# Kernel tuning notes

Hardware: AMD Instinct MI355X
Metric: run time of the kernel (lower is better)

Reference implementation:

```python
import jax, jax.numpy as jnp
import numpy as np

N, M, C, L, T = 1024, 64, 512, 64, 8192
EPS = 1e-16


def setup_inputs() -> dict:
    key = jax.random.key(0)
    ks = jax.random.split(key, 9)
    sc = 0.05
    return {
        "sequence": jax.random.uniform(ks[0], (T, L), dtype=jnp.float32),
        "Wc": jax.random.normal(ks[1], (L + M, C), jnp.float32) * sc,
        "bc": jnp.zeros((C,), jnp.float32),
        "Wr": jax.random.normal(ks[2], (C, M + 6), jnp.float32) * sc,
        "br": jnp.zeros((M + 6,), jnp.float32),
        "Ww": jax.random.normal(ks[3], (C, 3 * M + 6), jnp.float32) * sc,
        "bw": jnp.zeros((3 * M + 6,), jnp.float32),
        "Wo": jax.random.normal(ks[4], (M, L), jnp.float32) * sc,
        "bo": jnp.zeros((L,), jnp.float32),
    }


def _address(Mt, k, beta, g, sh, gamma, w_prev):
    # content addressing: cosine similarity of key against each memory row
    sim = (Mt @ k) / (jnp.linalg.norm(Mt, axis=1) * jnp.linalg.norm(k) + EPS)
    wc = jax.nn.softmax(beta * sim)                      # [N]
    wg = g * wc + (1.0 - g) * w_prev                     # interpolation
    # circular convolution with 3-tap shift kernel (-1, 0, +1)
    ws = sh[0] * jnp.roll(wg, 1) + sh[1] * wg + sh[2] * jnp.roll(wg, -1)
    wsh = ws ** gamma                                    # sharpening
    return wsh / (jnp.sum(wsh) + EPS)


def _head_params(o):
    k = jnp.tanh(o[:M])
    beta = jax.nn.softplus(o[M])
    g = jax.nn.sigmoid(o[M + 1])
    sh = jax.nn.softmax(o[M + 2:M + 5])
    gamma = 1.0 + jax.nn.softplus(o[M + 5])
    return k, beta, g, sh, gamma


def reference(sequence, Wc, bc, Wr, br, Ww, bw, Wo, bo):
    M0 = jnp.full((N, M), 1e-06, jnp.float32)            # memory_bias
    w0 = jnp.zeros((N,), jnp.float32).at[N // 2].set(1.0)  # weight_bias
    r0 = jnp.full((M,), 1e-06, jnp.float32)              # read_bias

    def step(carry, s):
        Mt, ww, rw, r = carry
        h = jnp.tanh(jnp.concatenate([s, r]) @ Wc + bc)  # controller
        # write head: k, beta, g, shift, gamma, erase, add
        ow = h @ Ww + bw
        k, beta, g, sh, gamma = _head_params(ow)
        e = jax.nn.sigmoid(ow[M + 6:2 * M + 6])
        a = jnp.tanh(ow[2 * M + 6:])
        ww_n = _address(Mt, k, beta, g, sh, gamma, ww)
        Mt = Mt * (1.0 - ww_n[:, None] * e[None, :]) + ww_n[:, None] * a[None, :]
        # read head
        orr = h @ Wr + br
        k, beta, g, sh, gamma = _head_params(orr)
        rw_n = _address(Mt, k, beta, g, sh, gamma, rw)
        r_n = rw_n @ Mt                                  # [M]
        s_out = jnp.clip(r_n @ Wo + bo, 0.0, 1.0)
        return (Mt, ww_n, rw_n, r_n), (s_out, ww_n, rw_n, a, r_n)

    _, (seq_out, ww_h, rw_h, a_h, r_h) = jax.lax.scan(step, (M0, w0, w0, r0), sequence)
    return seq_out, ww_h, rw_h, a_h, r_h
```

## Files before the change

kernel.cpp:

```cpp
#include <hip/hip_runtime.h>
#include <math.h>

#define NN 1024
#define MM 64
#define CC 512
#define LL 64
#define TT 8192
#define EPSF 1e-16f

#define OFF_SEQ 0
#define OFF_WW  (TT*LL)
#define OFF_RW  (OFF_WW + TT*NN)
#define OFF_A   (OFF_RW + TT*NN)
#define OFF_R   (OFF_A + TT*MM)

#define WSF_PRE   0
#define WSF_M     (TT*CC)
#define WSF_WCAT  (WSF_M + 32768)

#define BAR() asm volatile("s_waitcnt lgkmcnt(0)\n\ts_barrier" ::: "memory")

__device__ __forceinline__ float sigmoid_f(float x) { return 1.0f / (1.0f + __expf(-x)); }
__device__ __forceinline__ float softplus_f(float x) { return (x > 15.0f) ? x : __logf(1.0f + __expf(x)); }
__device__ __forceinline__ float tanh_f(float x) { float e = __expf(2.0f * x); return 1.0f - 2.0f / (e + 1.0f); }
__device__ __forceinline__ float pow_f(float b, float g) { return __expf(g * __logf(b)); }
__device__ __forceinline__ int bitrev4(int l) {
    return ((l & 1) << 3) | ((l & 2) << 1) | ((l & 4) >> 1) | ((l & 8) >> 3);
}

__device__ __forceinline__ float xor_any(float v, const int m, const int lane) {
    if (m == 1)
        return __int_as_float(__builtin_amdgcn_mov_dpp(__float_as_int(v), 0xB1, 0xF, 0xF, true));
    if (m == 2)
        return __int_as_float(__builtin_amdgcn_mov_dpp(__float_as_int(v), 0x4E, 0xF, 0xF, true));
    return __shfl_xor(v, m, 64);
}

__device__ __forceinline__ float bfly64(float s, const int lane) {
    s += xor_any(s, 1, lane);
    s += xor_any(s, 2, lane);
    s += xor_any(s, 4, lane);
    s += xor_any(s, 8, lane);
    s += xor_any(s, 16, lane);
    s += xor_any(s, 32, lane);
    return s;
}

__global__ void pre_kernel(const float* __restrict__ seq, const float* __restrict__ Wc,
                           const float* __restrict__ bc, float* __restrict__ pre) {
    int gid = blockIdx.x * blockDim.x + threadIdx.x;
    int t = gid >> 9;
    int j = gid & 511;
    if (t >= TT) return;
    const float* s = seq + t * LL;
    float acc = bc[j];
    #pragma unroll 8
    for (int i = 0; i < LL; ++i) acc += s[i] * Wc[i * CC + j];
    pre[gid] = acc;
}

__global__ void pack_kernel(const float* __restrict__ Ww, const float* __restrict__ Wr,
                            float* __restrict__ Wcat) {
    int gid = blockIdx.x * 256 + threadIdx.x;
    if (gid >= 512 * 272) return;
    int r = gid / 272, c = gid - r * 272;
    float v = 0.0f;
    if (c < 198) v = Ww[r * 198 + c];
    else if (c < 268) v = Wr[r * 70 + (c - 198)];
    Wcat[gid] = v;
}

__global__ __launch_bounds__(1024)
void ntm_kernel(
    const float* __restrict__ pre,
    const float* __restrict__ Wc,
    const float* __restrict__ Wcat,
    const float* __restrict__ br,
    const float* __restrict__ bw,
    const float* __restrict__ Wo,
    const float* __restrict__ bo,
    float* __restrict__ out)
{
    __shared__ __align__(16) float sh_part[4096];
    __shared__ __align__(16) float sh_h[CC];
    __shared__ __align__(16) float sh_kw[MM];
    __shared__ __align__(16) float sh_kr[MM];
    __shared__ __align__(16) float sh_e[MM];
    __shared__ __align__(16) float sh_a[MM];
    __shared__ __align__(16) float sh_scal[16];
    __shared__ __align__(16) float sh_evbuf[NN];
    __shared__ __align__(16) float sh_wpbuf[NN];
    __shared__ __align__(16) float red[4][16];
    __shared__ __align__(16) float wmat[16][MM];
    __shared__ __align__(16) float sh_r[MM];
    __shared__ __align__(16) float sh_WoT[LL * MM];
    __shared__ __align__(16) float sh_bo[LL];
    __shared__ __align__(16) float sh_bw[200];
    __shared__ __align__(16) float sh_br[72];
    __shared__ __align__(16) float sh_pren[CC];

    const int tid  = threadIdx.x;
    const int lane = tid & 63;
    const int wv   = tid >> 6;

    for (int idx = tid; idx < MM * LL; idx += NN) {
        int i = idx >> 6, o = idx & 63;
        sh_WoT[o * MM + i] = Wo[i * LL + o];
    }
    if (tid < LL)  sh_bo[tid] = bo[tid];
    if (tid < 198) sh_bw[tid] = bw[tid];
    if (tid < 70)  sh_br[tid] = br[tid];
    if (tid < MM)  sh_r[tid] = 1e-6f;
    if (tid < CC)  sh_pren[tid] = pre[tid];

    float Mlo[32];
    #pragma unroll
    for (int j = 0; j < 32; ++j) Mlo[j] = 1e-6f;
    float4 mh[8];
    #pragma unroll
    for (int k = 0; k < 8; ++k) mh[k] = make_float4(1e-6f, 1e-6f, 1e-6f, 1e-6f);
    float rown = sqrtf(64.0f * 1e-12f);
    float wwprev = (tid == NN / 2) ? 1.0f : 0.0f;
    float rwprev = wwprev;
    __syncthreads();

    for (int t = 0; t < TT; ++t) {
        {
            int g = tid & 127, q = tid >> 7;
            const float4* wbase = (const float4*)(Wc + (64 + q * 8) * CC) + g;
            float4 ra = *(const float4*)(sh_r + q * 8);
            float4 rb = *(const float4*)(sh_r + q * 8 + 4);
            float rv[8] = {ra.x, ra.y, ra.z, ra.w, rb.x, rb.y, rb.z, rb.w};
            float4 acc = make_float4(0.0f, 0.0f, 0.0f, 0.0f);
            #pragma unroll
            for (int i = 0; i < 8; ++i) {
                float4 w = wbase[i * 128];
                acc.x += rv[i] * w.x; acc.y += rv[i] * w.y;
                acc.z += rv[i] * w.z; acc.w += rv[i] * w.w;
            }
            ((float4*)sh_part)[q * 128 + g] = acc;
        }
        BAR();
        if (tid < CC) {
            float p0 = sh_part[tid]          + sh_part[512 + tid];
            float p1 = sh_part[1024 + tid]   + sh_part[1536 + tid];
            float p2 = sh_part[2048 + tid]   + sh_part[2560 + tid];
            float p3 = sh_part[3072 + tid]   + sh_part[3584 + tid];
            float v = sh_pren[tid] + ((p0 + p1) + (p2 + p3));
            sh_h[tid] = tanh_f(v);
        }
        BAR();
        if (tid < 544) {
            int g = tid % 68, q = tid / 68;
            const float4* wbase = (const float4*)(Wcat + (q * 64) * 272) + g;
            const float4* h4p = (const float4*)(sh_h + q * 64);
            float4 acc = make_float4(0.0f, 0.0f, 0.0f, 0.0f);
            #pragma unroll 2
            for (int i4 = 0; i4 < 16; ++i4) {
                float4 h4 = h4p[i4];
                const float4* wr = wbase + (i4 * 4) * 68;
                float4 w0 = wr[0];
                float4 w1 = wr[68];
                float4 w2 = wr[136];
                float4 w3 = wr[204];
                acc.x += h4.x * w0.x; acc.y += h4.x * w0.y; acc.z += h4.x * w0.z; acc.w += h4.x * w0.w;
                acc.x += h4.y * w1.x; acc.y += h4.y * w1.y; acc.z += h4.y * w1.z; acc.w += h4.y * w1.w;
                acc.x += h4.z * w2.x; acc.y += h4.z * w2.y; acc.z += h4.z * w2.z; acc.w += h4.z * w2.w;
                acc.x += h4.w * w3.x; acc.y += h4.w * w3.y; acc.z += h4.w * w3.z; acc.w += h4.w * w3.w;
            }
            ((float4*)sh_part)[q * 68 + g] = acc;
        }
        BAR();
        float pren_v = 0.0f;
        #define OWV(c) ( (((sh_part[(c)] + sh_part[272 + (c)]) + (sh_part[544 + (c)] + sh_part[816 + (c)])) \
                        + ((sh_part[1088 + (c)] + sh_part[1360 + (c)]) + (sh_part[1632 + (c)] + sh_part[1904 + (c)]))) \
                        + ((c) < 198 ? sh_bw[(c)] : sh_br[(c) - 198]) )
        if (wv == 0) {
            float v = tanh_f(OWV(lane));
            sh_kw[lane] = v;
            float s2 = bfly64(v * v, lane);
            if (lane == 0) sh_scal[6] = sqrtf(s2);
        } else if (wv == 1) {
            float v = tanh_f(OWV(198 + lane));
            sh_kr[lane] = v;
            float s2 = bfly64(v * v, lane);
            if (lane == 0) sh_scal[14] = sqrtf(s2);
        } else if (wv == 2) {
            sh_e[lane] = sigmoid_f(OWV(70 + lane));
        } else if (wv == 3) {
            float v = tanh_f(OWV(134 + lane));
            sh_a[lane] = v;
            out[OFF_A + t * MM + lane] = v;
        } else if (wv == 4) {
            if (lane == 0) {
                sh_scal[0] = softplus_f(OWV(64));
                sh_scal[1] = sigmoid_f(OWV(65));
                float x0 = OWV(66), x1 = OWV(67), x2 = OWV(68);
                float mx = fmaxf(x0, fmaxf(x1, x2));
                float e0 = __expf(x0 - mx), e1 = __expf(x1 - mx), e2 = __expf(x2 - mx);
                float ss = e0 + e1 + e2;
                sh_scal[2] = e0 / ss; sh_scal[3] = e1 / ss; sh_scal[4] = e2 / ss;
                sh_scal[5] = 1.0f + softplus_f(OWV(69));
            }
        } else if (wv == 5) {
            if (lane == 0) {
                sh_scal[8] = softplus_f(OWV(198 + 64));
                sh_scal[9] = sigmoid_f(OWV(198 + 65));
                float x0 = OWV(198 + 66), x1 = OWV(198 + 67), x2 = OWV(198 + 68);
                float mx = fmaxf(x0, fmaxf(x1, x2));
                float e0 = __expf(x0 - mx), e1 = __expf(x1 - mx), e2 = __expf(x2 - mx);
                float ss = e0 + e1 + e2;
                sh_scal[10] = e0 / ss; sh_scal[11] = e1 / ss; sh_scal[12] = e2 / ss;
                sh_scal[13] = 1.0f + softplus_f(OWV(198 + 69));
            }
        } else if (wv >= 6 && wv < 14) {
            if (t + 1 < TT) pren_v = pre[(t + 1) * CC + (tid - 384)];
        } else if (wv == 15) {
            if (t > 0) {
                const float4* r4p = (const float4*)sh_r;
                const float4* wop = (const float4*)(sh_WoT + lane * MM);
                float a0 = 0.0f, a1 = 0.0f;
                #pragma unroll
                for (int i4 = 0; i4 < 16; ++i4) {
                    float4 r = r4p[i4];
                    float4 w = wop[i4];
                    a0 += r.x * w.x + r.y * w.y;
                    a1 += r.z * w.z + r.w * w.w;
                }
                float acc = sh_bo[lane] + a0 + a1;
                out[OFF_SEQ + (t - 1) * LL + lane] = fminf(fmaxf(acc, 0.0f), 1.0f);
            }
        }
        #undef OWV
        BAR();

        float betaW = sh_scal[0], gW = sh_scal[1];
        float s0W = sh_scal[2], s1W = sh_scal[3], s2W = sh_scal[4];
        float gamW = sh_scal[5], knW = sh_scal[6];
        {
            const float4* k4 = (const float4*)sh_kw;
            float d0 = 0.0f, d1 = 0.0f, d2 = 0.0f, d3 = 0.0f;
            #pragma unroll
            for (int j4 = 0; j4 < 8; ++j4) {
                float4 k = k4[j4];
                d0 += Mlo[4*j4]   * k.x;
                d1 += Mlo[4*j4+1] * k.y;
                d2 += Mlo[4*j4+2] * k.z;
                d3 += Mlo[4*j4+3] * k.w;
            }
            #pragma unroll
            for (int k8 = 0; k8 < 8; ++k8) {
                float4 k = k4[8 + k8];
                d0 += mh[k8].x * k.x;
                d1 += mh[k8].y * k.y;
                d2 += mh[k8].z * k.z;
                d3 += mh[k8].w * k.w;
            }
            float dot = (d0 + d1) + (d2 + d3);
            float sim = dot / (rown * knW + EPSF);
            float ev = __expf(betaW * sim);
            sh_evbuf[tid] = ev;
            sh_wpbuf[tid] = wwprev;
            float s = bfly64(ev, lane);
            if (lane == 0) red[0][wv] = s;
        }
        BAR();
        float wshW;
        {
            const float4* rp = (const float4*)red[0];
            float Sev = 0.0f;
            #pragma unroll
            for (int w4 = 0; w4 < 4; ++w4) { float4 p = rp[w4]; Sev += p.x + p.y + p.z + p.w; }
            int tm1 = (tid + NN - 1) & (NN - 1), tp1 = (tid + 1) & (NN - 1);
            float cEV = s0W * sh_evbuf[tm1] + s1W * sh_evbuf[tid] + s2W * sh_evbuf[tp1];
            float cWP = s0W * sh_wpbuf[tm1] + s1W * sh_wpbuf[tid] + s2W * sh_wpbuf[tp1];
            float ws = (gW / Sev) * cEV + (1.0f - gW) * cWP;
            wshW = pow_f(ws, gamW);
            float s = bfly64(wshW, lane);
            if (lane == 0) red[1][wv] = s;
        }
        BAR();
        {
            const float4* rp = (const float4*)red[1];
            float Swsh = 0.0f;
            #pragma unroll
            for (int w4 = 0; w4 < 4; ++w4) { float4 p = rp[w4]; Swsh += p.x + p.y + p.z + p.w; }
            float wwn = wshW / (Swsh + EPSF);
            out[OFF_WW + t * NN + tid] = wwn;
            wwprev = wwn;
            const float4* e4p = (const float4*)sh_e;
            const float4* a4p = (const float4*)sh_a;
            float n0 = 0.0f, n1 = 0.0f, n2 = 0.0f, n3 = 0.0f;
            #pragma unroll
            for (int j4 = 0; j4 < 8; ++j4) {
                float4 e = e4p[j4], a = a4p[j4];
                float m0 = Mlo[4*j4]   * (1.0f - wwn * e.x) + wwn * a.x;
                float m1 = Mlo[4*j4+1] * (1.0f - wwn * e.y) + wwn * a.y;
                float m2 = Mlo[4*j4+2] * (1.0f - wwn * e.z) + wwn * a.z;
                float m3 = Mlo[4*j4+3] * (1.0f - wwn * e.w) + wwn * a.w;
                Mlo[4*j4] = m0; Mlo[4*j4+1] = m1; Mlo[4*j4+2] = m2; Mlo[4*j4+3] = m3;
                n0 += m0 * m0; n1 += m1 * m1; n2 += m2 * m2; n3 += m3 * m3;
            }
            #pragma unroll
            for (int k = 0; k < 8; ++k) {
                float4 e = e4p[8 + k], a = a4p[8 + k];
                float4 m = mh[k];
                m.x = m.x * (1.0f - wwn * e.x) + wwn * a.x;
                m.y = m.y * (1.0f - wwn * e.y) + wwn * a.y;
                m.z = m.z * (1.0f - wwn * e.z) + wwn * a.z;
                m.w = m.w * (1.0f - wwn * e.w) + wwn * a.w;
                mh[k] = m;
                n0 += m.x * m.x; n1 += m.y * m.y; n2 += m.z * m.z; n3 += m.w * m.w;
            }
            rown = sqrtf((n0 + n1) + (n2 + n3));
        }

        float betaR = sh_scal[8], gR = sh_scal[9];
        float s0R = sh_scal[10], s1R = sh_scal[11], s2R = sh_scal[12];
        float gamR = sh_scal[13], knR = sh_scal[14];
        {
            const float4* k4 = (const float4*)sh_kr;
            float d0 = 0.0f, d1 = 0.0f, d2 = 0.0f, d3 = 0.0f;
            #pragma unroll
            for (int j4 = 0; j4 < 8; ++j4) {
                float4 k = k4[j4];
                d0 += Mlo[4*j4]   * k.x;
                d1 += Mlo[4*j4+1] * k.y;
                d2 += Mlo[4*j4+2] * k.z;
                d3 += Mlo[4*j4+3] * k.w;
            }
            #pragma unroll
            for (int k8 = 0; k8 < 8; ++k8) {
                float4 k = k4[8 + k8];
                d0 += mh[k8].x * k.x;
                d1 += mh[k8].y * k.y;
                d2 += mh[k8].z * k.z;
                d3 += mh[k8].w * k.w;
            }
            float dot = (d0 + d1) + (d2 + d3);
            float sim = dot / (rown * knR + EPSF);
            float ev = __expf(betaR * sim);
            sh_evbuf[tid] = ev;
            sh_wpbuf[tid] = rwprev;
            float s = bfly64(ev, lane);
            if (lane == 0) red[2][wv] = s;
        }
        BAR();
        float wshR;
        {
            const float4* rp = (const float4*)red[2];
            float Sev = 0.0f;
            #pragma unroll
            for (int w4 = 0; w4 < 4; ++w4) { float4 p = rp[w4]; Sev += p.x + p.y + p.z + p.w; }
            int tm1 = (tid + NN - 1) & (NN - 1), tp1 = (tid + 1) & (NN - 1);
            float cEV = s0R * sh_evbuf[tm1] + s1R * sh_evbuf[tid] + s2R * sh_evbuf[tp1];
            float cWP = s0R * sh_wpbuf[tm1] + s1R * sh_wpbuf[tid] + s2R * sh_wpbuf[tp1];
            float ws = (gR / Sev) * cEV + (1.0f - gR) * cWP;
            wshR = pow_f(ws, gamR);
            float s = bfly64(wshR, lane);
            if (lane == 0) red[3][wv] = s;
            #pragma unroll
            for (int chunk = 0; chunk < 4; ++chunk) {
                const int cb = chunk * 16;
                float v[16];
                if (chunk < 2) {
                    #pragma unroll
                    for (int i = 0; i < 16; ++i) v[i] = wshR * Mlo[chunk * 16 + i];
                } else {
                    #pragma unroll
                    for (int k = 0; k < 4; ++k) {
                        float4 m = mh[(chunk - 2) * 4 + k];
                        v[4*k]   = wshR * m.x;
                        v[4*k+1] = wshR * m.y;
                        v[4*k+2] = wshR * m.z;
                        v[4*k+3] = wshR * m.w;
                    }
                }
                #pragma unroll
                for (int st = 0; st < 4; ++st) {
                    const int m = 1 << st;
                    const int hs = 8 >> st;
                    bool hi = (lane & m) != 0;
                    #pragma unroll
                    for (int i = 0; i < 8; ++i) {
                        if (i < hs) {
                            float send = hi ? v[i] : v[i + hs];
                            float recv = xor_any(send, m, lane);
                            float keep = hi ? v[i + hs] : v[i];
                            v[i] = keep + recv;
                        }
                    }
                }
                float v0 = v[0];
                v0 += xor_any(v0, 16, lane);
                v0 += xor_any(v0, 32, lane);
                if (lane < 16) wmat[wv][cb + bitrev4(lane)] = v0;
            }
        }
        BAR();
        {
            if (wv >= 6 && wv < 14 && t + 1 < TT) sh_pren[tid - 384] = pren_v;
            const float4* rp = (const float4*)red[3];
            float Swsh = 0.0f;
            #pragma unroll
            for (int w4 = 0; w4 < 4; ++w4) { float4 p = rp[w4]; Swsh += p.x + p.y + p.z + p.w; }
            float inv = 1.0f / (Swsh + EPSF);
            float rwn = wshR * inv;
            out[OFF_RW + t * NN + tid] = rwn;
            rwprev = rwn;
            if (tid < MM) {
                float rv = 0.0f;
                #pragma unroll
                for (int w = 0; w < 16; ++w) rv += wmat[w][tid];
                rv *= inv;
                sh_r[tid] = rv;
                out[OFF_R + t * MM + tid] = rv;
            }
        }
        BAR();
    }

    if (tid < LL) {
        const float4* r4p = (const float4*)sh_r;
        const float4* wop = (const float4*)(sh_WoT + tid * MM);
        float a0 = 0.0f, a1 = 0.0f;
        #pragma unroll
        for (int i4 = 0; i4 < 16; ++i4) {
            float4 r = r4p[i4];
            float4 w = wop[i4];
            a0 += r.x * w.x + r.y * w.y;
            a1 += r.z * w.z + r.w * w.w;
        }
        float acc = sh_bo[tid] + a0 + a1;
        out[OFF_SEQ + (TT - 1) * LL + tid] = fminf(fmaxf(acc, 0.0f), 1.0f);
    }
}

extern "C" void kernel_launch(void* const* d_in, const int* in_sizes, int n_in,
                              void* d_out, int out_size, void* d_ws, size_t ws_size,
                              hipStream_t stream) {
    const float* seq = (const float*)d_in[0];
    const float* Wc  = (const float*)d_in[1];
    const float* bc  = (const float*)d_in[2];
    const float* Wr  = (const float*)d_in[3];
    const float* br  = (const float*)d_in[4];
    const float* Ww  = (const float*)d_in[5];
    const float* bw  = (const float*)d_in[6];
    const float* Wo  = (const float*)d_in[7];
    const float* bo  = (const float*)d_in[8];
    float* out = (float*)d_out;

    float* wsf  = (float*)d_ws;
    float* pre  = wsf + WSF_PRE;
    float* Wcat = wsf + WSF_WCAT;

    pre_kernel<<<(TT * CC) / 256, 256, 0, stream>>>(seq, Wc, bc, pre);
    pack_kernel<<<(512 * 272 + 255) / 256, 256, 0, stream>>>(Ww, Wr, Wcat);
    ntm_kernel<<<1, 1024, 0, stream>>>(pre, Wc, Wcat, br, bw, Wo, bo, out);
}
```

Measured before the change: 137.3 ms.

## Halve the block to 512 threads, each owning two memory rows

The single-block recurrent kernel now runs with 512 threads instead of 1024. Each thread keeps two memory rows (A and B) in registers and computes both rows' addressing, updates and read contributions. The Wc-recurrent and head-projection loops are remapped to the smaller block, the prefetch of the next controller pre-activation is vectorised into one wave, and the transposed Wo tile is padded. The aim is to cut barrier and synchronisation cost per step by having fewer waves, at the price of twice the serial work per thread and much higher register pressure. That pressure could spill to scratch given the __launch_bounds__(512, 2) hint.

```diff
diff --git a/kernel.cpp b/kernel.cpp
--- a/kernel.cpp
+++ b/kernel.cpp
@@ -70,7 +70,8 @@
     Wcat[gid] = v;
 }
 
-__global__ __launch_bounds__(1024)
+#define WOT_S 68
+__global__ __launch_bounds__(512, 2)
 void ntm_kernel(
     const float* __restrict__ pre,
     const float* __restrict__ Wc,
@@ -93,7 +94,7 @@
     __shared__ __align__(16) float red[4][16];
     __shared__ __align__(16) float wmat[16][MM];
     __shared__ __align__(16) float sh_r[MM];
-    __shared__ __align__(16) float sh_WoT[LL * MM];
+    __shared__ __align__(16) float sh_WoT[LL * WOT_S];
     __shared__ __align__(16) float sh_bo[LL];
     __shared__ __align__(16) float sh_bw[200];
     __shared__ __align__(16) float sh_br[72];
@@ -102,46 +103,56 @@
     const int tid  = threadIdx.x;
     const int lane = tid & 63;
     const int wv   = tid >> 6;
-
-    for (int idx = tid; idx < MM * LL; idx += NN) {
+    const int r0   = tid;
+    const int r1   = tid + 512;
+
+    for (int idx = tid; idx < MM * LL; idx += 512) {
         int i = idx >> 6, o = idx & 63;
-        sh_WoT[o * MM + i] = Wo[i * LL + o];
+        sh_WoT[o * WOT_S + i] = Wo[i * LL + o];
     }
     if (tid < LL)  sh_bo[tid] = bo[tid];
     if (tid < 198) sh_bw[tid] = bw[tid];
     if (tid < 70)  sh_br[tid] = br[tid];
     if (tid < MM)  sh_r[tid] = 1e-6f;
-    if (tid < CC)  sh_pren[tid] = pre[tid];
-
-    float Mlo[32];
+    sh_pren[tid] = pre[tid];
+
+    float MloA[32], MloB[32];
     #pragma unroll
-    for (int j = 0; j < 32; ++j) Mlo[j] = 1e-6f;
-    float4 mh[8];
+    for (int j = 0; j < 32; ++j) { MloA[j] = 1e-6f; MloB[j] = 1e-6f; }
+    float4 mhA[8], mhB[8];
     #pragma unroll
-    for (int k = 0; k < 8; ++k) mh[k] = make_float4(1e-6f, 1e-6f, 1e-6f, 1e-6f);
-    float rown = sqrtf(64.0f * 1e-12f);
-    float wwprev = (tid == NN / 2) ? 1.0f : 0.0f;
-    float rwprev = wwprev;
+    for (int k = 0; k < 8; ++k) {
+        mhA[k] = make_float4(1e-6f, 1e-6f, 1e-6f, 1e-6f);
+        mhB[k] = mhA[k];
+    }
+    float rownA = sqrtf(64.0f * 1e-12f), rownB = rownA;
+    float wwprevA = 0.0f;
+    float wwprevB = (tid == 0) ? 1.0f : 0.0f;
+    float rwprevA = wwprevA, rwprevB = wwprevB;
     __syncthreads();
 
     for (int t = 0; t < TT; ++t) {
         {
             int g = tid & 127, q = tid >> 7;
-            const float4* wbase = (const float4*)(Wc + (64 + q * 8) * CC) + g;
-            float4 ra = *(const float4*)(sh_r + q * 8);
-            float4 rb = *(const float4*)(sh_r + q * 8 + 4);
-            float rv[8] = {ra.x, ra.y, ra.z, ra.w, rb.x, rb.y, rb.z, rb.w};
-            float4 acc = make_float4(0.0f, 0.0f, 0.0f, 0.0f);
-            #pragma unroll
-            for (int i = 0; i < 8; ++i) {
-                float4 w = wbase[i * 128];
-                acc.x += rv[i] * w.x; acc.y += rv[i] * w.y;
-                acc.z += rv[i] * w.z; acc.w += rv[i] * w.w;
-            }
-            ((float4*)sh_part)[q * 128 + g] = acc;
-        }
-        BAR();
-        if (tid < CC) {
+            #pragma unroll
+            for (int c2 = 0; c2 < 2; ++c2) {
+                int qq = q + c2 * 4;
+                const float4* wbase = (const float4*)(Wc + (64 + qq * 8) * CC) + g;
+                float4 ra = *(const float4*)(sh_r + qq * 8);
+                float4 rb = *(const float4*)(sh_r + qq * 8 + 4);
+                float rv[8] = {ra.x, ra.y, ra.z, ra.w, rb.x, rb.y, rb.z, rb.w};
+                float4 acc = make_float4(0.0f, 0.0f, 0.0f, 0.0f);
+                #pragma unroll
+                for (int i = 0; i < 8; ++i) {
+                    float4 w = wbase[i * 128];
+                    acc.x += rv[i] * w.x; acc.y += rv[i] * w.y;
+                    acc.z += rv[i] * w.z; acc.w += rv[i] * w.w;
+                }
+                ((float4*)sh_part)[qq * 128 + g] = acc;
+            }
+        }
+        BAR();
+        {
             float p0 = sh_part[tid]          + sh_part[512 + tid];
             float p1 = sh_part[1024 + tid]   + sh_part[1536 + tid];
             float p2 = sh_part[2048 + tid]   + sh_part[2560 + tid];
@@ -150,8 +161,8 @@
             sh_h[tid] = tanh_f(v);
         }
         BAR();
-        if (tid < 544) {
-            int g = tid % 68, q = tid / 68;
+        for (int u = tid; u < 544; u += 512) {
+            int g = u % 68, q = u / 68;
             const float4* wbase = (const float4*)(Wcat + (q * 64) * 272) + g;
             const float4* h4p = (const float4*)(sh_h + q * 64);
             float4 acc = make_float4(0.0f, 0.0f, 0.0f, 0.0f);
@@ -171,7 +182,7 @@
             ((float4*)sh_part)[q * 68 + g] = acc;
         }
         BAR();
-        float pren_v = 0.0f;
+        float4 pren0, pren1;
         #define OWV(c) ( (((sh_part[(c)] + sh_part[272 + (c)]) + (sh_part[544 + (c)] + sh_part[816 + (c)])) \
                         + ((sh_part[1088 + (c)] + sh_part[1360 + (c)]) + (sh_part[1632 + (c)] + sh_part[1904 + (c)]))) \
                         + ((c) < 198 ? sh_bw[(c)] : sh_br[(c) - 198]) )
@@ -213,12 +224,16 @@
                 sh_scal[10] = e0 / ss; sh_scal[11] = e1 / ss; sh_scal[12] = e2 / ss;
                 sh_scal[13] = 1.0f + softplus_f(OWV(198 + 69));
             }
-        } else if (wv >= 6 && wv < 14) {
-            if (t + 1 < TT) pren_v = pre[(t + 1) * CC + (tid - 384)];
-        } else if (wv == 15) {
+        } else if (wv == 6) {
+            if (t + 1 < TT) {
+                const float4* p4 = (const float4*)(pre + (t + 1) * CC) + (tid - 384) * 2;
+                pren0 = p4[0];
+                pren1 = p4[1];
+            }
+        } else {
             if (t > 0) {
                 const float4* r4p = (const float4*)sh_r;
-                const float4* wop = (const float4*)(sh_WoT + lane * MM);
+                const float4* wop = (const float4*)(sh_WoT + lane * WOT_S);
                 float a0 = 0.0f, a1 = 0.0f;
                 #pragma unroll
                 for (int i4 = 0; i4 < 16; ++i4) {
@@ -239,45 +254,56 @@
         float gamW = sh_scal[5], knW = sh_scal[6];
         {
             const float4* k4 = (const float4*)sh_kw;
-            float d0 = 0.0f, d1 = 0.0f, d2 = 0.0f, d3 = 0.0f;
+            float a0 = 0.0f, a1 = 0.0f, a2 = 0.0f, a3 = 0.0f;
+            float b0 = 0.0f, b1 = 0.0f, b2 = 0.0f, b3 = 0.0f;
             #pragma unroll
             for (int j4 = 0; j4 < 8; ++j4) {
                 float4 k = k4[j4];
-                d0 += Mlo[4*j4]   * k.x;
-                d1 += Mlo[4*j4+1] * k.y;
-                d2 += Mlo[4*j4+2] * k.z;
-                d3 += Mlo[4*j4+3] * k.w;
+                a0 += MloA[4*j4]   * k.x; a1 += MloA[4*j4+1] * k.y;
+                a2 += MloA[4*j4+2] * k.z; a3 += MloA[4*j4+3] * k.w;
+                b0 += MloB[4*j4]   * k.x; b1 += MloB[4*j4+1] * k.y;
+                b2 += MloB[4*j4+2] * k.z; b3 += MloB[4*j4+3] * k.w;
             }
             #pragma unroll
             for (int k8 = 0; k8 < 8; ++k8) {
                 float4 k = k4[8 + k8];
-                d0 += mh[k8].x * k.x;
-                d1 += mh[k8].y * k.y;
-                d2 += mh[k8].z * k.z;
-                d3 += mh[k8].w * k.w;
-            }
-            float dot = (d0 + d1) + (d2 + d3);
-            float sim = dot / (rown * knW + EPSF);
-            float ev = __expf(betaW * sim);
-            sh_evbuf[tid] = ev;
-            sh_wpbuf[tid] = wwprev;
-            float s = bfly64(ev, lane);
-            if (lane == 0) red[0][wv] = s;
-        }
-        BAR();
-        float wshW;
+                a0 += mhA[k8].x * k.x; a1 += mhA[k8].y * k.y;
+                a2 += mhA[k8].z * k.z; a3 += mhA[k8].w * k.w;
+                b0 += mhB[k8].x * k.x; b1 += mhB[k8].y * k.y;
+                b2 += mhB[k8].z * k.z; b3 += mhB[k8].w * k.w;
+            }
+            float dotA = (a0 + a1) + (a2 + a3);
+            float dotB = (b0 + b1) + (b2 + b3);
+            float evA = __expf(betaW * (dotA / (rownA * knW + EPSF)));
+            float evB = __expf(betaW * (dotB / (rownB * knW + EPSF)));
+            sh_evbuf[r0] = evA; sh_evbuf[r1] = evB;
+            sh_wpbuf[r0] = wwprevA; sh_wpbuf[r1] = wwprevB;
+            float sA = bfly64(evA, lane);
+            if (lane == 0) red[0][wv] = sA;
+            float sB = bfly64(evB, lane);
+            if (lane == 0) red[0][wv + 8] = sB;
+        }
+        BAR();
+        float wshWA, wshWB;
         {
             const float4* rp = (const float4*)red[0];
             float Sev = 0.0f;
             #pragma unroll
             for (int w4 = 0; w4 < 4; ++w4) { float4 p = rp[w4]; Sev += p.x + p.y + p.z + p.w; }
-            int tm1 = (tid + NN - 1) & (NN - 1), tp1 = (tid + 1) & (NN - 1);
-            float cEV = s0W * sh_evbuf[tm1] + s1W * sh_evbuf[tid] + s2W * sh_evbuf[tp1];
-            float cWP = s0W * sh_wpbuf[tm1] + s1W * sh_wpbuf[tid] + s2W * sh_wpbuf[tp1];
-            float ws = (gW / Sev) * cEV + (1.0f - gW) * cWP;
-            wshW = pow_f(ws, gamW);
-            float s = bfly64(wshW, lane);
-            if (lane == 0) red[1][wv] = s;
+            int am1 = (r0 + NN - 1) & (NN - 1), ap1 = (r0 + 1) & (NN - 1);
+            float cEVa = s0W * sh_evbuf[am1] + s1W * sh_evbuf[r0] + s2W * sh_evbuf[ap1];
+            float cWPa = s0W * sh_wpbuf[am1] + s1W * sh_wpbuf[r0] + s2W * sh_wpbuf[ap1];
+            float wsA = (gW / Sev) * cEVa + (1.0f - gW) * cWPa;
+            wshWA = pow_f(wsA, gamW);
+            int bm1 = (r1 + NN - 1) & (NN - 1), bp1 = (r1 + 1) & (NN - 1);
+            float cEVb = s0W * sh_evbuf[bm1] + s1W * sh_evbuf[r1] + s2W * sh_evbuf[bp1];
+            float cWPb = s0W * sh_wpbuf[bm1] + s1W * sh_wpbuf[r1] + s2W * sh_wpbuf[bp1];
+            float wsB = (gW / Sev) * cEVb + (1.0f - gW) * cWPb;
+            wshWB = pow_f(wsB, gamW);
+            float sA = bfly64(wshWA, lane);
+            if (lane == 0) red[1][wv] = sA;
+            float sB = bfly64(wshWB, lane);
+            if (lane == 0) red[1][wv + 8] = sB;
         }
         BAR();
         {
@@ -285,34 +311,51 @@
             float Swsh = 0.0f;
             #pragma unroll
             for (int w4 = 0; w4 < 4; ++w4) { float4 p = rp[w4]; Swsh += p.x + p.y + p.z + p.w; }
-            float wwn = wshW / (Swsh + EPSF);
-            out[OFF_WW + t * NN + tid] = wwn;
-            wwprev = wwn;
+            float wwnA = wshWA / (Swsh + EPSF);
+            float wwnB = wshWB / (Swsh + EPSF);
+            out[OFF_WW + t * NN + r0] = wwnA;
+            out[OFF_WW + t * NN + r1] = wwnB;
+            wwprevA = wwnA; wwprevB = wwnB;
             const float4* e4p = (const float4*)sh_e;
             const float4* a4p = (const float4*)sh_a;
-            float n0 = 0.0f, n1 = 0.0f, n2 = 0.0f, n3 = 0.0f;
+            float n0a = 0.0f, n1a = 0.0f, n2a = 0.0f, n3a = 0.0f;
+            float n0b = 0.0f, n1b = 0.0f, n2b = 0.0f, n3b = 0.0f;
             #pragma unroll
             for (int j4 = 0; j4 < 8; ++j4) {
                 float4 e = e4p[j4], a = a4p[j4];
-                float m0 = Mlo[4*j4]   * (1.0f - wwn * e.x) + wwn * a.x;
-                float m1 = Mlo[4*j4+1] * (1.0f - wwn * e.y) + wwn * a.y;
-                float m2 = Mlo[4*j4+2] * (1.0f - wwn * e.z) + wwn * a.z;
-                float m3 = Mlo[4*j4+3] * (1.0f - wwn * e.w) + wwn * a.w;
-                Mlo[4*j4] = m0; Mlo[4*j4+1] = m1; Mlo[4*j4+2] = m2; Mlo[4*j4+3] = m3;
-                n0 += m0 * m0; n1 += m1 * m1; n2 += m2 * m2; n3 += m3 * m3;
+                float m0 = MloA[4*j4]   * (1.0f - wwnA * e.x) + wwnA * a.x;
+                float m1 = MloA[4*j4+1] * (1.0f - wwnA * e.y) + wwnA * a.y;
+                float m2 = MloA[4*j4+2] * (1.0f - wwnA * e.z) + wwnA * a.z;
+                float m3 = MloA[4*j4+3] * (1.0f - wwnA * e.w) + wwnA * a.w;
+                MloA[4*j4] = m0; MloA[4*j4+1] = m1; MloA[4*j4+2] = m2; MloA[4*j4+3] = m3;
+                n0a += m0 * m0; n1a += m1 * m1; n2a += m2 * m2; n3a += m3 * m3;
+                float p0 = MloB[4*j4]   * (1.0f - wwnB * e.x) + wwnB * a.x;
+                float p1 = MloB[4*j4+1] * (1.0f - wwnB * e.y) + wwnB * a.y;
+                float p2 = MloB[4*j4+2] * (1.0f - wwnB * e.z) + wwnB * a.z;
+                float p3 = MloB[4*j4+3] * (1.0f - wwnB * e.w) + wwnB * a.w;
+                MloB[4*j4] = p0; MloB[4*j4+1] = p1; MloB[4*j4+2] = p2; MloB[4*j4+3] = p3;
+                n0b += p0 * p0; n1b += p1 * p1; n2b += p2 * p2; n3b += p3 * p3;
             }
             #pragma unroll
             for (int k = 0; k < 8; ++k) {
                 float4 e = e4p[8 + k], a = a4p[8 + k];
-                float4 m = mh[k];
-                m.x = m.x * (1.0f - wwn * e.x) + wwn * a.x;
-                m.y = m.y * (1.0f - wwn * e.y) + wwn * a.y;
-                m.z = m.z * (1.0f - wwn * e.z) + wwn * a.z;
-                m.w = m.w * (1.0f - wwn * e.w) + wwn * a.w;
-                mh[k] = m;
-                n0 += m.x * m.x; n1 += m.y * m.y; n2 += m.z * m.z; n3 += m.w * m.w;
-            }
-            rown = sqrtf((n0 + n1) + (n2 + n3));
+                float4 m = mhA[k];
+                m.x = m.x * (1.0f - wwnA * e.x) + wwnA * a.x;
+                m.y = m.y * (1.0f - wwnA * e.y) + wwnA * a.y;
+                m.z = m.z * (1.0f - wwnA * e.z) + wwnA * a.z;
+                m.w = m.w * (1.0f - wwnA * e.w) + wwnA * a.w;
+                mhA[k] = m;
+                n0a += m.x * m.x; n1a += m.y * m.y; n2a += m.z * m.z; n3a += m.w * m.w;
+                float4 p = mhB[k];
+                p.x = p.x * (1.0f - wwnB * e.x) + wwnB * a.x;
+                p.y = p.y * (1.0f - wwnB * e.y) + wwnB * a.y;
+                p.z = p.z * (1.0f - wwnB * e.z) + wwnB * a.z;
+                p.w = p.w * (1.0f - wwnB * e.w) + wwnB * a.w;
+                mhB[k] = p;
+                n0b += p.x * p.x; n1b += p.y * p.y; n2b += p.z * p.z; n3b += p.w * p.w;
+            }
+            rownA = sqrtf((n0a + n1a) + (n2a + n3a));
+            rownB = sqrtf((n0b + n1b) + (n2b + n3b));
         }
 
         float betaR = sh_scal[8], gR = sh_scal[9];
@@ -320,94 +363,118 @@
         float gamR = sh_scal[13], knR = sh_scal[14];
         {
             const float4* k4 = (const float4*)sh_kr;
-            float d0 = 0.0f, d1 = 0.0f, d2 = 0.0f, d3 = 0.0f;
+            float a0 = 0.0f, a1 = 0.0f, a2 = 0.0f, a3 = 0.0f;
+            float b0 = 0.0f, b1 = 0.0f, b2 = 0.0f, b3 = 0.0f;
             #pragma unroll
             for (int j4 = 0; j4 < 8; ++j4) {
                 float4 k = k4[j4];
-                d0 += Mlo[4*j4]   * k.x;
-                d1 += Mlo[4*j4+1] * k.y;
-                d2 += Mlo[4*j4+2] * k.z;
-                d3 += Mlo[4*j4+3] * k.w;
+                a0 += MloA[4*j4]   * k.x; a1 += MloA[4*j4+1] * k.y;
+                a2 += MloA[4*j4+2] * k.z; a3 += MloA[4*j4+3] * k.w;
+                b0 += MloB[4*j4]   * k.x; b1 += MloB[4*j4+1] * k.y;
+                b2 += MloB[4*j4+2] * k.z; b3 += MloB[4*j4+3] * k.w;
             }
             #pragma unroll
             for (int k8 = 0; k8 < 8; ++k8) {
                 float4 k = k4[8 + k8];
-                d0 += mh[k8].x * k.x;
-                d1 += mh[k8].y * k.y;
-                d2 += mh[k8].z * k.z;
-                d3 += mh[k8].w * k.w;
-            }
-            float dot = (d0 + d1) + (d2 + d3);
-            float sim = dot / (rown * knR + EPSF);
-            float ev = __expf(betaR * sim);
-            sh_evbuf[tid] = ev;
-            sh_wpbuf[tid] = rwprev;
-            float s = bfly64(ev, lane);
-            if (lane == 0) red[2][wv] = s;
-        }
-        BAR();
-        float wshR;
+                a0 += mhA[k8].x * k.x; a1 += mhA[k8].y * k.y;
+                a2 += mhA[k8].z * k.z; a3 += mhA[k8].w * k.w;
+                b0 += mhB[k8].x * k.x; b1 += mhB[k8].y * k.y;
+                b2 += mhB[k8].z * k.z; b3 += mhB[k8].w * k.w;
+            }
+            float dotA = (a0 + a1) + (a2 + a3);
+            float dotB = (b0 + b1) + (b2 + b3);
+            float evA = __expf(betaR * (dotA / (rownA * knR + EPSF)));
+            float evB = __expf(betaR * (dotB / (rownB * knR + EPSF)));
+            sh_evbuf[r0] = evA; sh_evbuf[r1] = evB;
+            sh_wpbuf[r0] = rwprevA; sh_wpbuf[r1] = rwprevB;
+            float sA = bfly64(evA, lane);
+            if (lane == 0) red[2][wv] = sA;
+            float sB = bfly64(evB, lane);
+            if (lane == 0) red[2][wv + 8] = sB;
+        }
+        BAR();
+        float wshRA, wshRB;
         {
             const float4* rp = (const float4*)red[2];
             float Sev = 0.0f;
             #pragma unroll
             for (int w4 = 0; w4 < 4; ++w4) { float4 p = rp[w4]; Sev += p.x + p.y + p.z + p.w; }
-            int tm1 = (tid + NN - 1) & (NN - 1), tp1 = (tid + 1) & (NN - 1);
-            float cEV = s0R * sh_evbuf[tm1] + s1R * sh_evbuf[tid] + s2R * sh_evbuf[tp1];
-            float cWP = s0R * sh_wpbuf[tm1] + s1R * sh_wpbuf[tid] + s2R * sh_wpbuf[tp1];
-            float ws = (gR / Sev) * cEV + (1.0f - gR) * cWP;
-            wshR = pow_f(ws, gamR);
-            float s = bfly64(wshR, lane);
-            if (lane == 0) red[3][wv] = s;
-            #pragma unroll
-            for (int chunk = 0; chunk < 4; ++chunk) {
-                const int cb = chunk * 16;
-                float v[16];
-                if (chunk < 2) {
-                    #pragma unroll
-                    for (int i = 0; i < 16; ++i) v[i] = wshR * Mlo[chunk * 16 + i];
-                } else {
-                    #pragma unroll
-                    for (int k = 0; k < 4; ++k) {
-                        float4 m = mh[(chunk - 2) * 4 + k];
-                        v[4*k]   = wshR * m.x;
-                        v[4*k+1] = wshR * m.y;
-                        v[4*k+2] = wshR * m.z;
-                        v[4*k+3] = wshR * m.w;
-                    }
-                }
+            int am1 = (r0 + NN - 1) & (NN - 1), ap1 = (r0 + 1) & (NN - 1);
+            float cEVa = s0R * sh_evbuf[am1] + s1R * sh_evbuf[r0] + s2R * sh_evbuf[ap1];
+            float cWPa = s0R * sh_wpbuf[am1] + s1R * sh_wpbuf[r0] + s2R * sh_wpbuf[ap1];
+            float wsA = (gR / Sev) * cEVa + (1.0f - gR) * cWPa;
+            wshRA = pow_f(wsA, gamR);
+            int bm1 = (r1 + NN - 1) & (NN - 1), bp1 = (r1 + 1) & (NN - 1);
+            float cEVb = s0R * sh_evbuf[bm1] + s1R * sh_evbuf[r1] + s2R * sh_evbuf[bp1];
+            float cWPb = s0R * sh_wpbuf[bm1] + s1R * sh_wpbuf[r1] + s2R * sh_wpbuf[bp1];
+            float wsB = (gR / Sev) * cEVb + (1.0f - gR) * cWPb;
+            wshRB = pow_f(wsB, gamR);
+            float sA = bfly64(wshRA, lane);
+            if (lane == 0) red[3][wv] = sA;
+            float sB = bfly64(wshRB, lane);
+            if (lane == 0) red[3][wv + 8] = sB;
+
+            #pragma unroll
+            for (int half = 0; half < 2; ++half) {
+                const int wrow = wv + half * 8;
+                const float wsh = half ? wshRB : wshRA;
                 #pragma unroll
-                for (int st = 0; st < 4; ++st) {
-                    const int m = 1 << st;
-                    const int hs = 8 >> st;
-                    bool hi = (lane & m) != 0;
-                    #pragma unroll
-                    for (int i = 0; i < 8; ++i) {
-                        if (i < hs) {
-                            float send = hi ? v[i] : v[i + hs];
-                            float recv = xor_any(send, m, lane);
-                            float keep = hi ? v[i + hs] : v[i];
-                            v[i] = keep + recv;
+                for (int chunk = 0; chunk < 4; ++chunk) {
+                    const int cb = chunk * 16;
+                    float v[16];
+                    if (chunk < 2) {
+                        #pragma unroll
+                        for (int i = 0; i < 16; ++i)
+                            v[i] = wsh * (half ? MloB[chunk * 16 + i] : MloA[chunk * 16 + i]);
+                    } else {
+                        #pragma unroll
+                        for (int k = 0; k < 4; ++k) {
+                            float4 m = half ? mhB[(chunk - 2) * 4 + k] : mhA[(chunk - 2) * 4 + k];
+                            v[4*k]   = wsh * m.x;
+                            v[4*k+1] = wsh * m.y;
+                            v[4*k+2] = wsh * m.z;
+                            v[4*k+3] = wsh * m.w;
                         }
                     }
+                    #pragma unroll
+                    for (int st = 0; st < 4; ++st) {
+                        const int m = 1 << st;
+                        const int hs = 8 >> st;
+                        bool hi = (lane & m) != 0;
+                        #pragma unroll
+                        for (int i = 0; i < 8; ++i) {
+                            if (i < hs) {
+                                float send = hi ? v[i] : v[i + hs];
+                                float recv = xor_any(send, m, lane);
+                                float keep = hi ? v[i + hs] : v[i];
+                                v[i] = keep + recv;
+                            }
+                        }
+                    }
+                    float v0 = v[0];
+                    v0 += xor_any(v0, 16, lane);
+                    v0 += xor_any(v0, 32, lane);
+                    if (lane < 16) wmat[wrow][cb + bitrev4(lane)] = v0;
                 }
-                float v0 = v[0];
-                v0 += xor_any(v0, 16, lane);
-                v0 += xor_any(v0, 32, lane);
-                if (lane < 16) wmat[wv][cb + bitrev4(lane)] = v0;
-            }
-        }
-        BAR();
-        {
-            if (wv >= 6 && wv < 14 && t + 1 < TT) sh_pren[tid - 384] = pren_v;
+            }
+        }
+        BAR();
+        {
+            if (wv == 6 && t + 1 < TT) {
+                float4* d4 = (float4*)sh_pren + (tid - 384) * 2;
+                d4[0] = pren0;
+                d4[1] = pren1;
+            }
             const float4* rp = (const float4*)red[3];
             float Swsh = 0.0f;
             #pragma unroll
             for (int w4 = 0; w4 < 4; ++w4) { float4 p = rp[w4]; Swsh += p.x + p.y + p.z + p.w; }
             float inv = 1.0f / (Swsh + EPSF);
-            float rwn = wshR * inv;
-            out[OFF_RW + t * NN + tid] = rwn;
-            rwprev = rwn;
+            float rwnA = wshRA * inv;
+            float rwnB = wshRB * inv;
+            out[OFF_RW + t * NN + r0] = rwnA;
+            out[OFF_RW + t * NN + r1] = rwnB;
+            rwprevA = rwnA; rwprevB = rwnB;
             if (tid < MM) {
                 float rv = 0.0f;
                 #pragma unroll
@@ -422,7 +489,7 @@
 
     if (tid < LL) {
         const float4* r4p = (const float4*)sh_r;
-        const float4* wop = (const float4*)(sh_WoT + tid * MM);
+        const float4* wop = (const float4*)(sh_WoT + tid * WOT_S);
         float a0 = 0.0f, a1 = 0.0f;
         #pragma unroll
         for (int i4 = 0; i4 < 16; ++i4) {
@@ -456,5 +523,5 @@
 
     pre_kernel<<<(TT * CC) / 256, 256, 0, stream>>>(seq, Wc, bc, pre);
     pack_kernel<<<(512 * 272 + 255) / 256, 256, 0, stream>>>(Ww, Wr, Wcat);
-    ntm_kernel<<<1, 1024, 0, stream>>>(pre, Wc, Wcat, br, bw, Wo, bo, out);
-}
+    ntm_kernel<<<1, 512, 0, stream>>>(pre, Wc, Wcat, br, bw, Wo, bo, out);
+}
```

Result: slower. 338.9 ms (+146.9%).
